# Kernel optimization log

Measured on AMD Instinct MI355X. Metric: run time of the kernel, lower is better.

## Reference

```python
import jax, jax.numpy as jnp
import numpy as np


def setup_inputs() -> dict:
    key = jax.random.key(0)
    b, l, d_model, n_head, topk = 2, 2048, 1024, 16, 32
    dh = d_model // n_head
    k0, k1, k2, k3, k4 = jax.random.split(key, 5)
    s = 1.0 / np.sqrt(d_model)
    return {
        "q_in": jax.random.normal(k0, (b, l, d_model), jnp.float32),
        "kv_in": jax.random.normal(k1, (b, l, d_model), jnp.float32),
        "w_q": jax.random.normal(k2, (d_model, d_model), jnp.float32) * s,
        "w_kv": jax.random.normal(k3, (d_model, 2 * dh), jnp.float32) * s,
        "w_concat": jax.random.normal(k4, (d_model, d_model), jnp.float32) * s,
        "topk": topk,
        "n_head": n_head,
    }


def _l2norm_seq(x):
    # F.normalize default dim=1 -> normalize along the sequence axis (faithful to source)
    n = jnp.sqrt(jnp.sum(x * x, axis=1, keepdims=True))
    return x / jnp.maximum(n, 1e-12)


def reference(q_in, kv_in, w_q, w_kv, w_concat, topk, n_head):
    b, l, d_model = q_in.shape
    dh = d_model // n_head
    scale = 1.0 / np.sqrt(dh)

    q = q_in @ w_q                                  # (b, l, d_model)
    kv = kv_in @ w_kv                               # (b, l, 2*dh)
    k, v = kv[..., :dh], kv[..., dh:]
    k, v = _l2norm_seq(k), _l2norm_seq(v)           # (b, l, dh) single shared KV head

    q = q.reshape(b, l, n_head, dh).transpose(0, 2, 1, 3)  # (b, h, l, dh)

    # one similarity matrix reused for local attention and kNN retrieval
    sims = jnp.einsum('bhld,bmd->bhlm', q, k)       # (b, h, l, m)

    # local SDPA (KV head broadcast over query heads)
    local = jnp.einsum('bhlm,bmd->bhld', jax.nn.softmax(sims * scale, axis=-1), v)

    # exact inner-product kNN over stored keys (faiss memory stores k only,
    # so retrieved key == retrieved value == nearest stored key vectors)
    _, idx = jax.lax.top_k(sims, topk)              # (b, h, l, topk)
    mem = jax.vmap(lambda kk, ii: kk[ii])(k, idx)   # (b, h, l, topk, dh)

    s_ret = jnp.einsum('bhld,bhltd->bhlt', q, mem) * scale
    retrieved = jnp.einsum('bhlt,bhltd->bhld', jax.nn.softmax(s_ret, axis=-1), mem)

    out = (local + retrieved).transpose(0, 2, 1, 3).reshape(b, l, d_model)
    return out @ w_concat
```

## Files before the change

### kernel.cpp

```cpp
#include <hip/hip_runtime.h>
#include <cstddef>
#include <cstring>

#define B_    2
#define L_    2048
#define DM_   1024
#define NH_   16
#define DH_   64
#define SCALE_ 0.125f

typedef __bf16 bf16x8 __attribute__((ext_vector_type(8)));
typedef float  f32x4  __attribute__((ext_vector_type(4)));
typedef unsigned short ushort8v __attribute__((ext_vector_type(8)));
typedef unsigned short ushort4v __attribute__((ext_vector_type(4)));
typedef unsigned long long u64;
typedef unsigned int u32;

__device__ __forceinline__ u32 flipf(float f) {
    u32 u = __float_as_uint(f);
    return (u & 0x80000000u) ? ~u : (u | 0x80000000u);
}
__device__ __forceinline__ float unflipf(u32 k) {
    u32 u = (k & 0x80000000u) ? (k ^ 0x80000000u) : ~k;
    return __uint_as_float(u);
}
__device__ __forceinline__ float bf2f(unsigned short u) {
    return __uint_as_float(((u32)u) << 16);
}
__device__ __forceinline__ unsigned short f2bf(float f) {
    __bf16 h = (__bf16)f;
    unsigned short u;
    __builtin_memcpy(&u, &h, 2);
    return u;
}

__global__ __launch_bounds__(256)
void wsplit3(const float* __restrict__ W, unsigned short* __restrict__ w1,
             unsigned short* __restrict__ w2, unsigned short* __restrict__ w3,
             int K, int N) {
    const int n0 = blockIdx.x << 6;
    const int k0 = blockIdx.y << 6;
    const int t  = threadIdx.x;
    __shared__ float s[64][65];
    const int rr = t >> 4;
    const int c4 = (t & 15) << 2;
    #pragma unroll
    for (int rep = 0; rep < 4; ++rep) {
        int k = rr + (rep << 4);
        float4 x = *(const float4*)(W + (size_t)(k0 + k) * N + n0 + c4);
        s[k][c4+0] = x.x; s[k][c4+1] = x.y; s[k][c4+2] = x.z; s[k][c4+3] = x.w;
    }
    __syncthreads();
    #pragma unroll
    for (int rep = 0; rep < 4; ++rep) {
        int n = rr + (rep << 4);
        ushort4v h, m, l;
        #pragma unroll
        for (int j = 0; j < 4; ++j) {
            float x = s[c4 + j][n];
            unsigned short hh = f2bf(x);
            float r = x - bf2f(hh);
            unsigned short mm = f2bf(r);
            float r2 = r - bf2f(mm);
            h[j] = hh; m[j] = mm; l[j] = f2bf(r2);
        }
        size_t o = (size_t)(n0 + n) * K + k0 + c4;
        *(ushort4v*)(w1 + o) = h;
        *(ushort4v*)(w2 + o) = m;
        *(ushort4v*)(w3 + o) = l;
    }
}

__global__ __launch_bounds__(256)
void gemm6p(const float* __restrict__ A, const unsigned short* __restrict__ w1,
            const unsigned short* __restrict__ w2, const unsigned short* __restrict__ w3,
            float* __restrict__ C, int N, int K) {
    __shared__ __align__(16) unsigned short sA[3][128][40];
    __shared__ __align__(16) unsigned short sW[3][64][40];
    const int t    = threadIdx.x;
    const int wv   = t >> 6;
    const int lane = t & 63;
    const int quad = lane >> 4;
    const int n15  = lane & 15;
    const int bm = blockIdx.y << 7;
    const int bn = blockIdx.x << 6;
    const int wm = (wv >> 1) << 6;
    const int wn = (wv & 1) << 5;
    f32x4 acc[4][2];
    #pragma unroll
    for (int i = 0; i < 4; ++i)
        #pragma unroll
        for (int j = 0; j < 2; ++j)
            #pragma unroll
            for (int r = 0; r < 4; ++r) acc[i][j][r] = 0.f;

    const int ar  = t >> 1,  acg = (t & 1) << 4;
    const int wr  = t >> 2,  wcg = (t & 3) << 3;
    const float* Ap = A + (size_t)(bm + ar) * K + acg;
    const size_t wo = (size_t)(bn + wr) * K + wcg;

    for (int k0 = 0; k0 < K; k0 += 32) {
        float4 a0 = *(const float4*)(Ap + k0);
        float4 a1 = *(const float4*)(Ap + k0 + 4);
        float4 a2 = *(const float4*)(Ap + k0 + 8);
        float4 a3 = *(const float4*)(Ap + k0 + 12);
        ushort8v u1 = *(const ushort8v*)(w1 + wo + k0);
        ushort8v u2 = *(const ushort8v*)(w2 + wo + k0);
        ushort8v u3 = *(const ushort8v*)(w3 + wo + k0);
        __syncthreads();
        {
            float av[16] = {a0.x,a0.y,a0.z,a0.w, a1.x,a1.y,a1.z,a1.w,
                            a2.x,a2.y,a2.z,a2.w, a3.x,a3.y,a3.z,a3.w};
            ushort8v h0, h1, m0, m1, lo0, lo1;
            #pragma unroll
            for (int i = 0; i < 8; ++i) {
                float x = av[i];
                unsigned short hh = f2bf(x);
                float r = x - bf2f(hh);
                unsigned short mm = f2bf(r);
                h0[i] = hh; m0[i] = mm; lo0[i] = f2bf(r - bf2f(mm));
                float y = av[8 + i];
                unsigned short hh2 = f2bf(y);
                float r2 = y - bf2f(hh2);
                unsigned short mm2 = f2bf(r2);
                h1[i] = hh2; m1[i] = mm2; lo1[i] = f2bf(r2 - bf2f(mm2));
            }
            *(ushort8v*)&sA[0][ar][acg]     = h0;
            *(ushort8v*)&sA[0][ar][acg + 8] = h1;
            *(ushort8v*)&sA[1][ar][acg]     = m0;
            *(ushort8v*)&sA[1][ar][acg + 8] = m1;
            *(ushort8v*)&sA[2][ar][acg]     = lo0;
            *(ushort8v*)&sA[2][ar][acg + 8] = lo1;
            *(ushort8v*)&sW[0][wr][wcg] = u1;
            *(ushort8v*)&sW[1][wr][wcg] = u2;
            *(ushort8v*)&sW[2][wr][wcg] = u3;
        }
        __syncthreads();
        bf16x8 af[3][4];
        #pragma unroll
        for (int mi = 0; mi < 4; ++mi) {
            af[0][mi] = *(const bf16x8*)&sA[0][wm + (mi << 4) + n15][quad << 3];
            af[1][mi] = *(const bf16x8*)&sA[1][wm + (mi << 4) + n15][quad << 3];
            af[2][mi] = *(const bf16x8*)&sA[2][wm + (mi << 4) + n15][quad << 3];
        }
        #pragma unroll
        for (int nj = 0; nj < 2; ++nj) {
            bf16x8 wf1 = *(const bf16x8*)&sW[0][wn + (nj << 4) + n15][quad << 3];
            bf16x8 wf2 = *(const bf16x8*)&sW[1][wn + (nj << 4) + n15][quad << 3];
            bf16x8 wf3 = *(const bf16x8*)&sW[2][wn + (nj << 4) + n15][quad << 3];
            #pragma unroll
            for (int mi = 0; mi < 4; ++mi) {
                acc[mi][nj] = __builtin_amdgcn_mfma_f32_16x16x32_bf16(af[0][mi], wf1, acc[mi][nj], 0, 0, 0);
                acc[mi][nj] = __builtin_amdgcn_mfma_f32_16x16x32_bf16(af[0][mi], wf2, acc[mi][nj], 0, 0, 0);
                acc[mi][nj] = __builtin_amdgcn_mfma_f32_16x16x32_bf16(af[1][mi], wf1, acc[mi][nj], 0, 0, 0);
                acc[mi][nj] = __builtin_amdgcn_mfma_f32_16x16x32_bf16(af[1][mi], wf2, acc[mi][nj], 0, 0, 0);
                acc[mi][nj] = __builtin_amdgcn_mfma_f32_16x16x32_bf16(af[0][mi], wf3, acc[mi][nj], 0, 0, 0);
                acc[mi][nj] = __builtin_amdgcn_mfma_f32_16x16x32_bf16(af[2][mi], wf1, acc[mi][nj], 0, 0, 0);
            }
        }
    }
    #pragma unroll
    for (int mi = 0; mi < 4; ++mi)
        #pragma unroll
        for (int nj = 0; nj < 2; ++nj)
            #pragma unroll
            for (int r = 0; r < 4; ++r)
                C[(size_t)(bm + wm + (mi << 4) + (quad << 2) + r) * N
                  + bn + wn + (nj << 4) + n15] = acc[mi][nj][r];
}

__global__ __launch_bounds__(256)
void gemm3p(const float* __restrict__ A, const unsigned short* __restrict__ w1,
            const unsigned short* __restrict__ w2,
            float* __restrict__ C, int N, int K) {
    __shared__ __align__(16) unsigned short sA[2][128][40];
    __shared__ __align__(16) unsigned short sW[2][64][40];
    const int t    = threadIdx.x;
    const int wv   = t >> 6;
    const int lane = t & 63;
    const int quad = lane >> 4;
    const int n15  = lane & 15;
    const int bm = blockIdx.y << 7;
    const int bn = blockIdx.x << 6;
    const int wm = (wv >> 1) << 6;
    const int wn = (wv & 1) << 5;
    f32x4 acc[4][2];
    #pragma unroll
    for (int i = 0; i < 4; ++i)
        #pragma unroll
        for (int j = 0; j < 2; ++j)
            #pragma unroll
            for (int r = 0; r < 4; ++r) acc[i][j][r] = 0.f;

    const int ar  = t >> 1,  acg = (t & 1) << 4;
    const int wr  = t >> 2,  wcg = (t & 3) << 3;
    const float* Ap = A + (size_t)(bm + ar) * K + acg;
    const size_t wo = (size_t)(bn + wr) * K + wcg;

    for (int k0 = 0; k0 < K; k0 += 32) {
        float4 a0 = *(const float4*)(Ap + k0);
        float4 a1 = *(const float4*)(Ap + k0 + 4);
        float4 a2 = *(const float4*)(Ap + k0 + 8);
        float4 a3 = *(const float4*)(Ap + k0 + 12);
        ushort8v u1 = *(const ushort8v*)(w1 + wo + k0);
        ushort8v u2 = *(const ushort8v*)(w2 + wo + k0);
        __syncthreads();
        {
            float av[16] = {a0.x,a0.y,a0.z,a0.w, a1.x,a1.y,a1.z,a1.w,
                            a2.x,a2.y,a2.z,a2.w, a3.x,a3.y,a3.z,a3.w};
            ushort8v h0, h1, l0v, l1v;
            #pragma unroll
            for (int i = 0; i < 8; ++i) {
                float x = av[i];
                unsigned short hh = f2bf(x);
                h0[i] = hh; l0v[i] = f2bf(x - bf2f(hh));
                float y = av[8 + i];
                unsigned short hh2 = f2bf(y);
                h1[i] = hh2; l1v[i] = f2bf(y - bf2f(hh2));
            }
            *(ushort8v*)&sA[0][ar][acg]     = h0;
            *(ushort8v*)&sA[0][ar][acg + 8] = h1;
            *(ushort8v*)&sA[1][ar][acg]     = l0v;
            *(ushort8v*)&sA[1][ar][acg + 8] = l1v;
            *(ushort8v*)&sW[0][wr][wcg] = u1;
            *(ushort8v*)&sW[1][wr][wcg] = u2;
        }
        __syncthreads();
        bf16x8 af[2][4];
        #pragma unroll
        for (int mi = 0; mi < 4; ++mi) {
            af[0][mi] = *(const bf16x8*)&sA[0][wm + (mi << 4) + n15][quad << 3];
            af[1][mi] = *(const bf16x8*)&sA[1][wm + (mi << 4) + n15][quad << 3];
        }
        #pragma unroll
        for (int nj = 0; nj < 2; ++nj) {
            bf16x8 wf1 = *(const bf16x8*)&sW[0][wn + (nj << 4) + n15][quad << 3];
            bf16x8 wf2 = *(const bf16x8*)&sW[1][wn + (nj << 4) + n15][quad << 3];
            #pragma unroll
            for (int mi = 0; mi < 4; ++mi) {
                acc[mi][nj] = __builtin_amdgcn_mfma_f32_16x16x32_bf16(af[0][mi], wf1, acc[mi][nj], 0, 0, 0);
                acc[mi][nj] = __builtin_amdgcn_mfma_f32_16x16x32_bf16(af[0][mi], wf2, acc[mi][nj], 0, 0, 0);
                acc[mi][nj] = __builtin_amdgcn_mfma_f32_16x16x32_bf16(af[1][mi], wf1, acc[mi][nj], 0, 0, 0);
            }
        }
    }
    #pragma unroll
    for (int mi = 0; mi < 4; ++mi)
        #pragma unroll
        for (int nj = 0; nj < 2; ++nj)
            #pragma unroll
            for (int r = 0; r < 4; ++r)
                C[(size_t)(bm + wm + (mi << 4) + (quad << 2) + r) * N
                  + bn + wn + (nj << 4) + n15] = acc[mi][nj][r];
}

__global__ __launch_bounds__(256)
void col_norms(const float* __restrict__ kv, float* __restrict__ invn) {
    const int bc = blockIdx.x;
    const int b  = bc >> 7;
    const int c  = bc & 127;
    const int t  = threadIdx.x;
    const float* base = kv + (size_t)b * L_ * 128 + c;
    float ss = 0.f;
    for (int l = t; l < L_; l += 256) {
        float x = base[(size_t)l * 128];
        ss += x * x;
    }
    #pragma unroll
    for (int off = 32; off; off >>= 1) ss += __shfl_xor(ss, off);
    __shared__ float red[4];
    if ((t & 63) == 0) red[t >> 6] = ss;
    __syncthreads();
    if (t == 0) {
        float tot = red[0] + red[1] + red[2] + red[3];
        invn[bc] = 1.f / fmaxf(sqrtf(tot), 1e-12f);
    }
}

__global__ __launch_bounds__(256)
void scale_kv(const float* __restrict__ kv, const float* __restrict__ invn,
              float* __restrict__ kn, __bf16* __restrict__ kh,
              __bf16* __restrict__ vT) {
    const int b  = blockIdx.y;
    const int l0 = blockIdx.x << 6;
    const int t  = threadIdx.x;
    __shared__ float s_inv[128];
    __shared__ float s_vt[64][65];
    if (t < 128) s_inv[t] = invn[b * 128 + t];
    __syncthreads();
    #pragma unroll
    for (int rep = 0; rep < 8; ++rep) {
        int idx = (rep << 8) + t;
        int li  = idx >> 5;
        int c4  = (idx & 31) << 2;
        float4 x = *(const float4*)(kv + ((size_t)(b * L_ + l0 + li)) * 128 + c4);
        x.x *= s_inv[c4]; x.y *= s_inv[c4+1]; x.z *= s_inv[c4+2]; x.w *= s_inv[c4+3];
        if (c4 < 64) {
            size_t o = ((size_t)(b * L_ + l0 + li)) * DH_ + c4;
            *(float4*)(kn + o) = x;
            kh[o+0] = (__bf16)x.x; kh[o+1] = (__bf16)x.y;
            kh[o+2] = (__bf16)x.z; kh[o+3] = (__bf16)x.w;
        } else {
            int d = c4 - 64;
            s_vt[d+0][li] = x.x; s_vt[d+1][li] = x.y; s_vt[d+2][li] = x.z; s_vt[d+3][li] = x.w;
        }
    }
    __syncthreads();
    #pragma unroll
    for (int rep = 0; rep < 4; ++rep) {
        int idx = (rep << 8) + t;
        int d   = idx >> 4;
        int j   = (idx & 15) << 2;
        size_t o = ((size_t)b * DH_ + d) * L_ + l0 + j;
        vT[o+0] = (__bf16)s_vt[d][j+0];
        vT[o+1] = (__bf16)s_vt[d][j+1];
        vT[o+2] = (__bf16)s_vt[d][j+2];
        vT[o+3] = (__bf16)s_vt[d][j+3];
    }
}

#define SST2_ 1032

__global__ __launch_bounds__(256, 4)
void attn_part(const float* __restrict__ q,
               const __bf16* __restrict__ kh,
               const __bf16* __restrict__ vT,
               float* __restrict__ attn,
               unsigned short* __restrict__ cand,
               int* __restrict__ candC) {
    const int tile = blockIdx.x;
    const int h    = blockIdx.y;
    const int b    = blockIdx.z;
    const int l0   = tile << 4;
    const int t    = threadIdx.x;
    const int w    = t >> 6;
    const int lane = t & 63;
    const int quad = lane >> 4;
    const int n15  = lane & 15;

    __shared__ unsigned short s_sims[16 * SST2_];
    __shared__ float s_local[16][66];
    __shared__ float s_denom[16];

    {
        float* sl = &s_local[0][0];
        for (int i = t; i < 16 * 66; i += 256) sl[i] = 0.f;
        if (t < 16) s_denom[t] = 0.f;
    }

    bf16x8 qf[2];
    {
        const float* qp = q + ((size_t)(b * L_ + l0 + n15)) * DM_ + h * DH_ + (quad << 3);
        #pragma unroll
        for (int ks = 0; ks < 2; ++ks) {
            float4 x0 = *(const float4*)(qp + (ks << 5));
            float4 x1 = *(const float4*)(qp + (ks << 5) + 4);
            float xv[8] = {x0.x, x0.y, x0.z, x0.w, x1.x, x1.y, x1.z, x1.w};
            #pragma unroll
            for (int i2 = 0; i2 < 8; ++i2) qf[ks][i2] = (__bf16)xv[i2];
        }
    }

    f32x4 accL[4] = {{0,0,0,0},{0,0,0,0},{0,0,0,0},{0,0,0,0}};
    float psum = 0.f;
    const __bf16* khb = kh + (size_t)b * L_ * DH_;
    const __bf16* vtb = vT + (size_t)b * DH_ * L_;
    const int rg0 = ((b * NH_ + h) * L_) + l0;

    #pragma unroll 1
    for (int hf = 0; hf < 2; ++hf) {
        #pragma unroll
        for (int g = 0; g < 4; ++g) {
            bf16x8 kf[8];
            const __bf16* kp = khb + (size_t)((hf << 10) + (w << 8) + (g << 6) + n15) * DH_ + (quad << 3);
            #pragma unroll
            for (int jj = 0; jj < 4; ++jj) {
                kf[2*jj]   = *(const bf16x8*)(kp + (size_t)(jj << 4) * DH_);
                kf[2*jj+1] = *(const bf16x8*)(kp + (size_t)(jj << 4) * DH_ + 32);
            }
            #pragma unroll
            for (int jj = 0; jj < 4; ++jj) {
                int m0 = (w << 8) + (g << 6) + (jj << 4);
                f32x4 acc = {0.f, 0.f, 0.f, 0.f};
                acc = __builtin_amdgcn_mfma_f32_16x16x32_bf16(qf[0], kf[2*jj],   acc, 0, 0, 0);
                acc = __builtin_amdgcn_mfma_f32_16x16x32_bf16(qf[1], kf[2*jj+1], acc, 0, 0, 0);
                #pragma unroll
                for (int rr = 0; rr < 4; ++rr)
                    s_sims[((quad << 2) + rr) * SST2_ + m0 + n15] = f2bf(acc[rr]);
            }
        }
        __syncthreads();

        #pragma unroll 1
        for (int rr2 = 0; rr2 < 4; ++rr2) {
            const int r = (w << 2) + rr2;
            const unsigned short* srow = s_sims + r * SST2_;
            ushort8v rv[2];
            rv[0] = *(const ushort8v*)(srow + (lane << 3));
            rv[1] = *(const ushort8v*)(srow + 512 + (lane << 3));
            float bv = -3e38f;
            #pragma unroll
            for (int j = 0; j < 2; ++j)
                #pragma unroll
                for (int e = 0; e < 8; ++e) bv = fmaxf(bv, bf2f(rv[j][e]));
            u32 key = flipf(bv);
            u32 thr = 0;
            #pragma unroll
            for (int bp = 31; bp >= 0; --bp) {
                u32 tt = thr | (1u << bp);
                if (__popcll(__ballot(key >= tt)) >= 32) thr = tt;
            }
            float thrv = unflipf(thr) - 0.01f;
            int base = 0;
            unsigned short* cr = cand + (size_t)(rg0 + r) * 192 + hf * 96;
            #pragma unroll
            for (int j = 0; j < 2; ++j) {
                #pragma unroll
                for (int e = 0; e < 8; ++e) {
                    bool pred = bf2f(rv[j][e]) >= thrv;
                    u64 mk = __ballot(pred);
                    if (pred) {
                        int pos = base + __popcll(mk & ((1ull << lane) - 1));
                        if (pos < 96)
                            cr[pos] = (unsigned short)((hf << 10) + (j << 9) + (lane << 3) + e);
                    }
                    base += __popcll(mk);
                }
            }
            if (lane == 0) candC[((rg0 + r) << 1) + hf] = base < 96 ? base : 96;
        }

        #pragma unroll
        for (int g = 0; g < 4; ++g) {
            bf16x8 bvv[2][4];
            #pragma unroll
            for (int t2 = 0; t2 < 2; ++t2)
                #pragma unroll
                for (int nn = 0; nn < 4; ++nn)
                    bvv[t2][nn] = *(const bf16x8*)(vtb + (size_t)((nn << 4) + n15) * L_
                                  + (hf << 10) + (w << 8) + (g << 6) + (t2 << 5) + (quad << 3));
            #pragma unroll
            for (int t2 = 0; t2 < 2; ++t2) {
                int mb = (w << 8) + (g << 6) + (t2 << 5);
                ushort8v pu = *(const ushort8v*)(s_sims + n15 * SST2_ + mb + (quad << 3));
                bf16x8 af;
                #pragma unroll
                for (int e = 0; e < 8; ++e) {
                    float p = __expf(SCALE_ * bf2f(pu[e]));
                    psum += p;
                    af[e] = (__bf16)p;
                }
                #pragma unroll
                for (int nn = 0; nn < 4; ++nn)
                    accL[nn] = __builtin_amdgcn_mfma_f32_16x16x32_bf16(af, bvv[t2][nn], accL[nn], 0, 0, 0);
            }
        }
        __syncthreads();
    }

    psum += __shfl_xor(psum, 16);
    psum += __shfl_xor(psum, 32);
    if (lane < 16) atomicAdd(&s_denom[lane], psum);
    #pragma unroll
    for (int nn = 0; nn < 4; ++nn)
        #pragma unroll
        for (int rr = 0; rr < 4; ++rr)
            atomicAdd(&s_local[(quad << 2) + rr][(nn << 4) + n15], accL[nn][rr]);
    __syncthreads();

    {
        int r  = t >> 4;
        int d0 = (t & 15) << 2;
        float inv = 1.f / s_denom[r];
        float* op = attn + ((size_t)(b * L_ + l0 + r)) * DM_ + h * DH_ + d0;
        op[0] = s_local[r][d0+0] * inv;
        op[1] = s_local[r][d0+1] * inv;
        op[2] = s_local[r][d0+2] * inv;
        op[3] = s_local[r][d0+3] * inv;
    }
}

__global__ __launch_bounds__(256)
void topk_merge(const float* __restrict__ q, const float* __restrict__ kn,
                const unsigned short* __restrict__ cand,
                const int* __restrict__ candC, float* __restrict__ attn) {
    const int wv   = threadIdx.x >> 6;
    const int lane = threadIdx.x & 63;
    const int row  = (blockIdx.x << 2) + wv;
    const int l = row & (L_ - 1);
    const int h = (row >> 11) & (NH_ - 1);
    const int b = row >> 15;
    __shared__ __align__(16) u64 s_sel[4][32];

    const int c0 = candC[row << 1];
    const int c1 = candC[(row << 1) + 1];
    const int C  = c0 + c1;
    const int nb = (C + 63) >> 6;
    const unsigned short* cr = cand + (size_t)row * 192;
    const float* knb = kn + (size_t)b * L_ * DH_;
    const float* qr  = q + ((size_t)(b * L_ + l)) * DM_ + h * DH_;

    float4 qx[16];
    #pragma unroll
    for (int d4 = 0; d4 < 16; ++d4) qx[d4] = *(const float4*)(qr + (d4 << 2));

    u32   keyv[3];
    float dotv[3];
    int   mv[3];
    #pragma unroll 1
    for (int bt = 0; bt < nb; ++bt) {
        int i = (bt << 6) + lane;
        bool act = i < C;
        int m = 0;
        if (act) m = (i < c0) ? (int)cr[i] : (int)cr[96 + (i - c0)];
        const float* kr = knb + (size_t)m * DH_;
        float4 kx[16];
        #pragma unroll
        for (int d4 = 0; d4 < 16; ++d4) kx[d4] = *(const float4*)(kr + (d4 << 2));
        float dot = 0.f;
        #pragma unroll
        for (int d4 = 0; d4 < 16; ++d4)
            dot += kx[d4].x * qx[d4].x + kx[d4].y * qx[d4].y
                 + kx[d4].z * qx[d4].z + kx[d4].w * qx[d4].w;
        keyv[bt] = act ? flipf(dot) : 0u;
        dotv[bt] = dot;
        mv[bt]   = m;
    }
    u32 thr2 = 0;
    #pragma unroll 1
    for (int bp = 31; bp >= 0; --bp) {
        u32 tt = thr2 | (1u << bp);
        int c2 = 0;
        for (int bt = 0; bt < nb; ++bt)
            c2 += __popcll(__ballot(keyv[bt] >= tt));
        if (c2 >= 32) thr2 = tt;
    }
    int off = 0;
    #pragma unroll 1
    for (int bt = 0; bt < nb; ++bt) {
        bool pred = keyv[bt] >= thr2;
        u64 mk = __ballot(pred);
        if (pred) {
            int pos = off + __popcll(mk & ((1ull << lane) - 1));
            if (pos < 32) {
                float pt = __expf(SCALE_ * dotv[bt]);
                s_sel[wv][pos] = ((u64)__float_as_uint(pt) << 32) | (u32)mv[bt];
            }
        }
        off += __popcll(mk);
    }
    {
        float pts[32];
        int   ms[32];
        #pragma unroll
        for (int i = 0; i < 32; ++i) {
            u64 s0 = s_sel[wv][i];
            pts[i] = __uint_as_float((u32)(s0 >> 32));
            ms[i]  = (int)(u32)(s0 & 0xffffffffu);
        }
        const float* knb2 = knb + lane;
        float kvv[32];
        #pragma unroll
        for (int i = 0; i < 32; ++i) kvv[i] = knb2[(size_t)ms[i] * DH_];
        float rs = 0.f, ret = 0.f;
        #pragma unroll
        for (int i = 0; i < 16; ++i) {
            rs  += pts[2*i] + pts[2*i+1];
            ret += pts[2*i] * kvv[2*i] + pts[2*i+1] * kvv[2*i+1];
        }
        size_t oa = ((size_t)(b * L_ + l)) * DM_ + h * DH_ + lane;
        attn[oa] = attn[oa] + ret / rs;
    }
}

extern "C" void kernel_launch(void* const* d_in, const int* in_sizes, int n_in,
                              void* d_out, int out_size, void* d_ws, size_t ws_size,
                              hipStream_t stream) {
    const float* q_in     = (const float*)d_in[0];
    const float* kv_in    = (const float*)d_in[1];
    const float* w_q      = (const float*)d_in[2];
    const float* w_kv     = (const float*)d_in[3];
    const float* w_concat = (const float*)d_in[4];
    float* out = (float*)d_out;

    float* ws   = (float*)d_ws;
    float* q    = ws;
    float* attn = ws + 4194304;
    float* kv   = attn;
    float* kn   = ws + 8388608;
    float* invn = ws + 8650752;
    unsigned short* us = (unsigned short*)(ws + 8651008);
    unsigned short* kh_u = us;
    unsigned short* vT_u = us + 262144;
    unsigned short* wq1  = us + 524288;
    unsigned short* wq2  = wq1 + 1048576;
    unsigned short* wq3  = wq2 + 1048576;
    unsigned short* wc1  = wq3 + 1048576;
    unsigned short* wc2  = wc1 + 1048576;
    unsigned short* wkv1 = wc2 + 1048576;
    unsigned short* wkv2 = wkv1 + 131072;
    unsigned short* wkv3 = wkv2 + 131072;
    unsigned short* cand = wkv3 + 131072;
    unsigned short* wc3  = cand;
    int* candC = (int*)(cand + 12582912);
    __bf16* kh = (__bf16*)kh_u;
    __bf16* vT = (__bf16*)vT_u;

    wsplit3<<<dim3(DM_ / 64, DM_ / 64), 256, 0, stream>>>(w_q, wq1, wq2, wq3, DM_, DM_);
    wsplit3<<<dim3(DM_ / 64, DM_ / 64), 256, 0, stream>>>(w_concat, wc1, wc2, wc3, DM_, DM_);
    wsplit3<<<dim3(128 / 64, DM_ / 64), 256, 0, stream>>>(w_kv, wkv1, wkv2, wkv3, DM_, 128);

    gemm6p<<<dim3(DM_ / 64, (B_ * L_) / 128), 256, 0, stream>>>(q_in, wq1, wq2, wq3, q, DM_, DM_);
    gemm6p<<<dim3(128 / 64, (B_ * L_) / 128), 256, 0, stream>>>(kv_in, wkv1, wkv2, wkv3, kv, 128, DM_);

    col_norms<<<B_ * 128, 256, 0, stream>>>(kv, invn);
    scale_kv<<<dim3(L_ / 64, B_), 256, 0, stream>>>(kv, invn, kn, kh, vT);

    attn_part<<<dim3(L_ / 16, NH_, B_), 256, 0, stream>>>(q, kh, vT, attn, cand, candC);
    topk_merge<<<(B_ * NH_ * L_) / 4, 256, 0, stream>>>(q, kn, cand, candC, attn);

    gemm3p<<<dim3(DM_ / 64, (B_ * L_) / 128), 256, 0, stream>>>(attn, wc1, wc2, out, DM_, DM_);
}
```

Measured before the change: 826.0 us.

## Merge top-k candidate halves in-kernel with packed bf16 scores and cooperative rescoring

The attention kernel now keeps a running row maximum across both key halves. In the second half it re-filters the first-half candidates against a combined threshold, so each row emits one candidate list of at most 96 entries instead of two lists of 96. Each candidate carries its bf16 similarity alongside the index, and the threshold radix search runs over 16 bits instead of 32. The sims tile is written with swapped MFMA operands so one 64-bit packed store replaces four scalar stores. The merge kernel rescores candidates cooperatively, with 16 lanes per key using float4 loads and shuffle reductions instead of a serial 64-float load per lane. This cuts candidate traffic and per-lane register pressure, at the cost of more branching and a tighter candidate cap that could drop true top-k entries near the threshold.

```diff
diff --git a/kernel.cpp b/kernel.cpp
--- a/kernel.cpp
+++ b/kernel.cpp
@@ -20,10 +20,6 @@
     u32 u = __float_as_uint(f);
     return (u & 0x80000000u) ? ~u : (u | 0x80000000u);
 }
-__device__ __forceinline__ float unflipf(u32 k) {
-    u32 u = (k & 0x80000000u) ? (k ^ 0x80000000u) : ~k;
-    return __uint_as_float(u);
-}
 __device__ __forceinline__ float bf2f(unsigned short u) {
     return __uint_as_float(((u32)u) << 16);
 }
@@ -32,6 +28,12 @@
     unsigned short u;
     __builtin_memcpy(&u, &h, 2);
     return u;
+}
+__device__ __forceinline__ u32 flip16(unsigned short u) {
+    return (u & 0x8000u) ? (u32)(~u & 0xffffu) : (u32)(u | 0x8000u);
+}
+__device__ __forceinline__ unsigned short unflip16(u32 k) {
+    return (k & 0x8000u) ? (unsigned short)(k ^ 0x8000u) : (unsigned short)(~k & 0xffffu);
 }
 
 __global__ __launch_bounds__(256)
@@ -326,7 +328,7 @@
                const __bf16* __restrict__ kh,
                const __bf16* __restrict__ vT,
                float* __restrict__ attn,
-               unsigned short* __restrict__ cand,
+               u32* __restrict__ cand,
                int* __restrict__ candC) {
     const int tile = blockIdx.x;
     const int h    = blockIdx.y;
@@ -363,6 +365,8 @@
 
     f32x4 accL[4] = {{0,0,0,0},{0,0,0,0},{0,0,0,0},{0,0,0,0}};
     float psum = 0.f;
+    float bvmax[4] = {-3e38f, -3e38f, -3e38f, -3e38f};
+    int   c0[4]    = {0, 0, 0, 0};
     const __bf16* khb = kh + (size_t)b * L_ * DH_;
     const __bf16* vtb = vT + (size_t)b * DH_ * L_;
     const int rg0 = ((b * NH_ + h) * L_) + l0;
@@ -382,11 +386,12 @@
             for (int jj = 0; jj < 4; ++jj) {
                 int m0 = (w << 8) + (g << 6) + (jj << 4);
                 f32x4 acc = {0.f, 0.f, 0.f, 0.f};
-                acc = __builtin_amdgcn_mfma_f32_16x16x32_bf16(qf[0], kf[2*jj],   acc, 0, 0, 0);
-                acc = __builtin_amdgcn_mfma_f32_16x16x32_bf16(qf[1], kf[2*jj+1], acc, 0, 0, 0);
-                #pragma unroll
-                for (int rr = 0; rr < 4; ++rr)
-                    s_sims[((quad << 2) + rr) * SST2_ + m0 + n15] = f2bf(acc[rr]);
+                acc = __builtin_amdgcn_mfma_f32_16x16x32_bf16(kf[2*jj],   qf[0], acc, 0, 0, 0);
+                acc = __builtin_amdgcn_mfma_f32_16x16x32_bf16(kf[2*jj+1], qf[1], acc, 0, 0, 0);
+                u32 lo = (u32)f2bf(acc[0]) | ((u32)f2bf(acc[1]) << 16);
+                u32 hi = (u32)f2bf(acc[2]) | ((u32)f2bf(acc[3]) << 16);
+                u64 pk = ((u64)hi << 32) | lo;
+                *(u64*)(s_sims + (size_t)n15 * SST2_ + m0 + (quad << 2)) = pk;
             }
         }
         __syncthreads();
@@ -403,31 +408,84 @@
             for (int j = 0; j < 2; ++j)
                 #pragma unroll
                 for (int e = 0; e < 8; ++e) bv = fmaxf(bv, bf2f(rv[j][e]));
-            u32 key = flipf(bv);
-            u32 thr = 0;
-            #pragma unroll
-            for (int bp = 31; bp >= 0; --bp) {
-                u32 tt = thr | (1u << bp);
-                if (__popcll(__ballot(key >= tt)) >= 32) thr = tt;
-            }
-            float thrv = unflipf(thr) - 0.01f;
-            int base = 0;
-            unsigned short* cr = cand + (size_t)(rg0 + r) * 192 + hf * 96;
-            #pragma unroll
-            for (int j = 0; j < 2; ++j) {
-                #pragma unroll
-                for (int e = 0; e < 8; ++e) {
-                    bool pred = bf2f(rv[j][e]) >= thrv;
+            bvmax[rr2] = fmaxf(bvmax[rr2], bv);
+            u32* cr = cand + (size_t)(rg0 + r) * 96;
+            if (hf == 0) {
+                u32 key = flip16(f2bf(bv));
+                u32 thr = 0;
+                #pragma unroll
+                for (int bp = 15; bp >= 0; --bp) {
+                    u32 tt = thr | (1u << bp);
+                    if (__popcll(__ballot(key >= tt)) >= 32) thr = tt;
+                }
+                float thrv = bf2f(unflip16(thr)) - 0.01f;
+                int base = 0;
+                #pragma unroll
+                for (int j = 0; j < 2; ++j) {
+                    #pragma unroll
+                    for (int e = 0; e < 8; ++e) {
+                        bool pred = bf2f(rv[j][e]) >= thrv;
+                        u64 mk = __ballot(pred);
+                        if (pred) {
+                            int pos = base + __popcll(mk & ((1ull << lane) - 1));
+                            if (pos < 96)
+                                cr[pos] = ((u32)rv[j][e] << 16)
+                                        | (u32)((j << 9) + (lane << 3) + e);
+                        }
+                        base += __popcll(mk);
+                    }
+                }
+                c0[rr2] = base < 96 ? base : 96;
+            } else {
+                u32 key = flip16(f2bf(bvmax[rr2]));
+                u32 thr = 0;
+                #pragma unroll
+                for (int bp = 15; bp >= 0; --bp) {
+                    u32 tt = thr | (1u << bp);
+                    if (__popcll(__ballot(key >= tt)) >= 32) thr = tt;
+                }
+                float thrv = bf2f(unflip16(thr)) - 0.01f;
+                const int cc0 = c0[rr2];
+                u32 e0 = (lane < cc0) ? cr[lane] : 0u;
+                u32 e1 = (64 + lane < cc0) ? cr[64 + lane] : 0u;
+                int base = 0;
+                {
+                    bool pred = (lane < cc0)
+                              && (bf2f((unsigned short)(e0 >> 16)) >= thrv);
+                    u64 mk = __ballot(pred);
+                    if (pred) {
+                        int pos = __popcll(mk & ((1ull << lane) - 1));
+                        cr[pos] = e0;
+                    }
+                    base = __popcll(mk);
+                }
+                if (cc0 > 64) {
+                    bool pred = (64 + lane < cc0)
+                              && (bf2f((unsigned short)(e1 >> 16)) >= thrv);
                     u64 mk = __ballot(pred);
                     if (pred) {
                         int pos = base + __popcll(mk & ((1ull << lane) - 1));
-                        if (pos < 96)
-                            cr[pos] = (unsigned short)((hf << 10) + (j << 9) + (lane << 3) + e);
+                        if (pos < 96) cr[pos] = e1;
                     }
                     base += __popcll(mk);
                 }
-            }
-            if (lane == 0) candC[((rg0 + r) << 1) + hf] = base < 96 ? base : 96;
+                #pragma unroll
+                for (int j = 0; j < 2; ++j) {
+                    #pragma unroll
+                    for (int e = 0; e < 8; ++e) {
+                        bool pred = bf2f(rv[j][e]) >= thrv;
+                        u64 mk = __ballot(pred);
+                        if (pred) {
+                            int pos = base + __popcll(mk & ((1ull << lane) - 1));
+                            if (pos < 96)
+                                cr[pos] = ((u32)rv[j][e] << 16)
+                                        | (u32)(1024 + (j << 9) + (lane << 3) + e);
+                        }
+                        base += __popcll(mk);
+                    }
+                }
+                if (lane == 0) candC[rg0 + r] = base < 96 ? base : 96;
+            }
         }
 
         #pragma unroll
@@ -482,72 +540,87 @@
 
 __global__ __launch_bounds__(256)
 void topk_merge(const float* __restrict__ q, const float* __restrict__ kn,
-                const unsigned short* __restrict__ cand,
-                const int* __restrict__ candC, float* __restrict__ attn) {
+                const u32* __restrict__ cand, const int* __restrict__ candC,
+                float* __restrict__ attn) {
     const int wv   = threadIdx.x >> 6;
     const int lane = threadIdx.x & 63;
     const int row  = (blockIdx.x << 2) + wv;
     const int l = row & (L_ - 1);
     const int h = (row >> 11) & (NH_ - 1);
     const int b = row >> 15;
+    __shared__ float s_dot[4][96];
     __shared__ __align__(16) u64 s_sel[4][32];
 
-    const int c0 = candC[row << 1];
-    const int c1 = candC[(row << 1) + 1];
-    const int C  = c0 + c1;
-    const int nb = (C + 63) >> 6;
-    const unsigned short* cr = cand + (size_t)row * 192;
+    const int C = candC[row];
+    const u32* cr = cand + (size_t)row * 96;
     const float* knb = kn + (size_t)b * L_ * DH_;
     const float* qr  = q + ((size_t)(b * L_ + l)) * DM_ + h * DH_;
 
-    float4 qx[16];
-    #pragma unroll
-    for (int d4 = 0; d4 < 16; ++d4) qx[d4] = *(const float4*)(qr + (d4 << 2));
-
-    u32   keyv[3];
-    float dotv[3];
-    int   mv[3];
-    #pragma unroll 1
-    for (int bt = 0; bt < nb; ++bt) {
-        int i = (bt << 6) + lane;
-        bool act = i < C;
-        int m = 0;
-        if (act) m = (i < c0) ? (int)cr[i] : (int)cr[96 + (i - c0)];
-        const float* kr = knb + (size_t)m * DH_;
-        float4 kx[16];
-        #pragma unroll
-        for (int d4 = 0; d4 < 16; ++d4) kx[d4] = *(const float4*)(kr + (d4 << 2));
-        float dot = 0.f;
-        #pragma unroll
-        for (int d4 = 0; d4 < 16; ++d4)
-            dot += kx[d4].x * qx[d4].x + kx[d4].y * qx[d4].y
-                 + kx[d4].z * qx[d4].z + kx[d4].w * qx[d4].w;
-        keyv[bt] = act ? flipf(dot) : 0u;
-        dotv[bt] = dot;
-        mv[bt]   = m;
-    }
+    int mreg0 = (lane < C) ? (int)(cr[lane] & 0xffffu) : 0;
+    int mreg1 = (64 + lane < C) ? (int)(cr[64 + lane] & 0xffffu) : 0;
+
+    const int cg = lane >> 4;
+    const int dg = lane & 15;
+    float4 qx = *(const float4*)(qr + (dg << 2));
+
+    #pragma unroll 2
+    for (int base = 0; base < C; base += 4) {
+        int ci = base + cg;
+        int src = ci & 63;
+        int mA = __shfl(mreg0, src);
+        int mB = __shfl(mreg1, src);
+        int m  = (ci < 64) ? mA : mB;
+        float4 kx = *(const float4*)(knb + (size_t)m * DH_ + (dg << 2));
+        float p = kx.x * qx.x + kx.y * qx.y + kx.z * qx.z + kx.w * qx.w;
+        p += __shfl_xor(p, 1);
+        p += __shfl_xor(p, 2);
+        p += __shfl_xor(p, 4);
+        p += __shfl_xor(p, 8);
+        if (dg == 0 && ci < C) s_dot[wv][ci] = p;
+    }
+
+    float dotA = (lane < C) ? s_dot[wv][lane] : 0.f;
+    float dotB = (64 + lane < C) ? s_dot[wv][64 + lane] : 0.f;
+    u32 keyA = (lane < C) ? flipf(dotA) : 0u;
+    u32 keyB = (64 + lane < C) ? flipf(dotB) : 0u;
+
     u32 thr2 = 0;
-    #pragma unroll 1
-    for (int bp = 31; bp >= 0; --bp) {
-        u32 tt = thr2 | (1u << bp);
-        int c2 = 0;
-        for (int bt = 0; bt < nb; ++bt)
-            c2 += __popcll(__ballot(keyv[bt] >= tt));
-        if (c2 >= 32) thr2 = tt;
-    }
-    int off = 0;
-    #pragma unroll 1
-    for (int bt = 0; bt < nb; ++bt) {
-        bool pred = keyv[bt] >= thr2;
-        u64 mk = __ballot(pred);
-        if (pred) {
-            int pos = off + __popcll(mk & ((1ull << lane) - 1));
+    if (C <= 64) {
+        #pragma unroll
+        for (int bp = 31; bp >= 0; --bp) {
+            u32 tt = thr2 | (1u << bp);
+            if (__popcll(__ballot(keyA >= tt)) >= 32) thr2 = tt;
+        }
+    } else {
+        #pragma unroll
+        for (int bp = 31; bp >= 0; --bp) {
+            u32 tt = thr2 | (1u << bp);
+            int c2 = __popcll(__ballot(keyA >= tt)) + __popcll(__ballot(keyB >= tt));
+            if (c2 >= 32) thr2 = tt;
+        }
+    }
+    {
+        bool pA = keyA >= thr2;
+        u64 mkA = __ballot(pA);
+        if (pA) {
+            int pos = __popcll(mkA & ((1ull << lane) - 1));
             if (pos < 32) {
-                float pt = __expf(SCALE_ * dotv[bt]);
-                s_sel[wv][pos] = ((u64)__float_as_uint(pt) << 32) | (u32)mv[bt];
-            }
-        }
-        off += __popcll(mk);
+                float pt = __expf(SCALE_ * dotA);
+                s_sel[wv][pos] = ((u64)__float_as_uint(pt) << 32) | (u32)mreg0;
+            }
+        }
+        if (C > 64) {
+            int cA = __popcll(mkA);
+            bool pB = keyB >= thr2;
+            u64 mkB = __ballot(pB);
+            if (pB) {
+                int pos = cA + __popcll(mkB & ((1ull << lane) - 1));
+                if (pos < 32) {
+                    float pt = __expf(SCALE_ * dotB);
+                    s_sel[wv][pos] = ((u64)__float_as_uint(pt) << 32) | (u32)mreg1;
+                }
+            }
+        }
     }
     {
         float pts[32];
@@ -600,9 +673,9 @@
     unsigned short* wkv1 = wc2 + 1048576;
     unsigned short* wkv2 = wkv1 + 131072;
     unsigned short* wkv3 = wkv2 + 131072;
-    unsigned short* cand = wkv3 + 131072;
-    unsigned short* wc3  = cand;
-    int* candC = (int*)(cand + 12582912);
+    u32* cand = (u32*)(wkv3 + 131072);
+    unsigned short* wc3 = (unsigned short*)cand;
+    int* candC = (int*)(cand + 65536 * 96);
     __bf16* kh = (__bf16*)kh_u;
     __bf16* vT = (__bf16*)vT_u;
 
```

Measured after the change: 688.3 us. 1.2x faster.

## Widen attention blocks to 512 threads and parallelize candidate scoring in top-k merge

Applied to the files above, without the earlier changes.

attn_part now runs 8 waves per block, each covering half as many keys and rows. It also packs the MFMA outputs into 64-bit shared stores by swapping operand order, and builds the candidate threshold on a 16-bit bf16 key using a running max across halves. Candidate compaction switches from per-element ballots to a per-lane bitmask with a wave prefix scan. topk_merge spreads each candidate dot product across 16 lanes with shuffle reductions and stages the results in shared memory, replacing the serial 64-wide per-lane dot. The goal is less ballot and register pressure and better latency hiding, at the cost of extra shuffles and a changed threshold heuristic that could alter which candidates are kept.

```diff
diff --git a/kernel.cpp b/kernel.cpp
--- a/kernel.cpp
+++ b/kernel.cpp
@@ -20,10 +20,6 @@
     u32 u = __float_as_uint(f);
     return (u & 0x80000000u) ? ~u : (u | 0x80000000u);
 }
-__device__ __forceinline__ float unflipf(u32 k) {
-    u32 u = (k & 0x80000000u) ? (k ^ 0x80000000u) : ~k;
-    return __uint_as_float(u);
-}
 __device__ __forceinline__ float bf2f(unsigned short u) {
     return __uint_as_float(((u32)u) << 16);
 }
@@ -32,6 +28,12 @@
     unsigned short u;
     __builtin_memcpy(&u, &h, 2);
     return u;
+}
+__device__ __forceinline__ u32 flip16(unsigned short u) {
+    return (u & 0x8000u) ? (u32)(~u & 0xffffu) : (u32)(u | 0x8000u);
+}
+__device__ __forceinline__ unsigned short unflip16(u32 k) {
+    return (k & 0x8000u) ? (unsigned short)(k ^ 0x8000u) : (unsigned short)(~k & 0xffffu);
 }
 
 __global__ __launch_bounds__(256)
@@ -321,7 +323,7 @@
 
 #define SST2_ 1032
 
-__global__ __launch_bounds__(256, 4)
+__global__ __launch_bounds__(512, 8)
 void attn_part(const float* __restrict__ q,
                const __bf16* __restrict__ kh,
                const __bf16* __restrict__ vT,
@@ -344,7 +346,7 @@
 
     {
         float* sl = &s_local[0][0];
-        for (int i = t; i < 16 * 66; i += 256) sl[i] = 0.f;
+        for (int i = t; i < 16 * 66; i += 512) sl[i] = 0.f;
         if (t < 16) s_denom[t] = 0.f;
     }
 
@@ -363,6 +365,7 @@
 
     f32x4 accL[4] = {{0,0,0,0},{0,0,0,0},{0,0,0,0},{0,0,0,0}};
     float psum = 0.f;
+    float bvmax[2] = {-3e38f, -3e38f};
     const __bf16* khb = kh + (size_t)b * L_ * DH_;
     const __bf16* vtb = vT + (size_t)b * DH_ * L_;
     const int rg0 = ((b * NH_ + h) * L_) + l0;
@@ -370,9 +373,9 @@
     #pragma unroll 1
     for (int hf = 0; hf < 2; ++hf) {
         #pragma unroll
-        for (int g = 0; g < 4; ++g) {
+        for (int g = 0; g < 2; ++g) {
             bf16x8 kf[8];
-            const __bf16* kp = khb + (size_t)((hf << 10) + (w << 8) + (g << 6) + n15) * DH_ + (quad << 3);
+            const __bf16* kp = khb + (size_t)((hf << 10) + (w << 7) + (g << 6) + n15) * DH_ + (quad << 3);
             #pragma unroll
             for (int jj = 0; jj < 4; ++jj) {
                 kf[2*jj]   = *(const bf16x8*)(kp + (size_t)(jj << 4) * DH_);
@@ -380,20 +383,21 @@
             }
             #pragma unroll
             for (int jj = 0; jj < 4; ++jj) {
-                int m0 = (w << 8) + (g << 6) + (jj << 4);
+                int m0 = (w << 7) + (g << 6) + (jj << 4);
                 f32x4 acc = {0.f, 0.f, 0.f, 0.f};
-                acc = __builtin_amdgcn_mfma_f32_16x16x32_bf16(qf[0], kf[2*jj],   acc, 0, 0, 0);
-                acc = __builtin_amdgcn_mfma_f32_16x16x32_bf16(qf[1], kf[2*jj+1], acc, 0, 0, 0);
-                #pragma unroll
-                for (int rr = 0; rr < 4; ++rr)
-                    s_sims[((quad << 2) + rr) * SST2_ + m0 + n15] = f2bf(acc[rr]);
+                acc = __builtin_amdgcn_mfma_f32_16x16x32_bf16(kf[2*jj],   qf[0], acc, 0, 0, 0);
+                acc = __builtin_amdgcn_mfma_f32_16x16x32_bf16(kf[2*jj+1], qf[1], acc, 0, 0, 0);
+                u32 lo = (u32)f2bf(acc[0]) | ((u32)f2bf(acc[1]) << 16);
+                u32 hi = (u32)f2bf(acc[2]) | ((u32)f2bf(acc[3]) << 16);
+                u64 pk = ((u64)hi << 32) | lo;
+                *(u64*)(s_sims + (size_t)n15 * SST2_ + m0 + (quad << 2)) = pk;
             }
         }
         __syncthreads();
 
         #pragma unroll 1
-        for (int rr2 = 0; rr2 < 4; ++rr2) {
-            const int r = (w << 2) + rr2;
+        for (int rr2 = 0; rr2 < 2; ++rr2) {
+            const int r = (w << 1) + rr2;
             const unsigned short* srow = s_sims + r * SST2_;
             ushort8v rv[2];
             rv[0] = *(const ushort8v*)(srow + (lane << 3));
@@ -403,45 +407,57 @@
             for (int j = 0; j < 2; ++j)
                 #pragma unroll
                 for (int e = 0; e < 8; ++e) bv = fmaxf(bv, bf2f(rv[j][e]));
-            u32 key = flipf(bv);
+            bvmax[rr2] = fmaxf(bvmax[rr2], bv);
+            u32 key = flip16(f2bf(hf == 0 ? bv : bvmax[rr2]));
             u32 thr = 0;
             #pragma unroll
-            for (int bp = 31; bp >= 0; --bp) {
+            for (int bp = 15; bp >= 0; --bp) {
                 u32 tt = thr | (1u << bp);
                 if (__popcll(__ballot(key >= tt)) >= 32) thr = tt;
             }
-            float thrv = unflipf(thr) - 0.01f;
-            int base = 0;
+            float thrv = bf2f(unflip16(thr)) - 0.01f;
+            u32 m16 = 0;
+            #pragma unroll
+            for (int j = 0; j < 2; ++j)
+                #pragma unroll
+                for (int e = 0; e < 8; ++e)
+                    if (bf2f(rv[j][e]) >= thrv) m16 |= 1u << ((j << 3) + e);
+            int c = __popc(m16);
+            int incl = c;
+            #pragma unroll
+            for (int off = 1; off < 64; off <<= 1) {
+                int v2 = __shfl_up(incl, off);
+                if (lane >= off) incl += v2;
+            }
+            int total = __shfl(incl, 63);
+            int pos = incl - c;
             unsigned short* cr = cand + (size_t)(rg0 + r) * 192 + hf * 96;
-            #pragma unroll
-            for (int j = 0; j < 2; ++j) {
-                #pragma unroll
-                for (int e = 0; e < 8; ++e) {
-                    bool pred = bf2f(rv[j][e]) >= thrv;
-                    u64 mk = __ballot(pred);
-                    if (pred) {
-                        int pos = base + __popcll(mk & ((1ull << lane) - 1));
-                        if (pos < 96)
-                            cr[pos] = (unsigned short)((hf << 10) + (j << 9) + (lane << 3) + e);
-                    }
-                    base += __popcll(mk);
-                }
-            }
-            if (lane == 0) candC[((rg0 + r) << 1) + hf] = base < 96 ? base : 96;
-        }
-
-        #pragma unroll
-        for (int g = 0; g < 4; ++g) {
+            u32 mm = m16;
+            while (mm) {
+                int e  = __ffs(mm) - 1;
+                mm &= mm - 1;
+                int j  = e >> 3;
+                int ee = e & 7;
+                if (pos < 96)
+                    cr[pos] = (unsigned short)((hf << 10) + (j << 9) + (lane << 3) + ee);
+                ++pos;
+            }
+            if (lane == 0)
+                candC[((rg0 + r) << 1) + hf] = total < 96 ? total : 96;
+        }
+
+        #pragma unroll
+        for (int g = 0; g < 2; ++g) {
             bf16x8 bvv[2][4];
             #pragma unroll
             for (int t2 = 0; t2 < 2; ++t2)
                 #pragma unroll
                 for (int nn = 0; nn < 4; ++nn)
                     bvv[t2][nn] = *(const bf16x8*)(vtb + (size_t)((nn << 4) + n15) * L_
-                                  + (hf << 10) + (w << 8) + (g << 6) + (t2 << 5) + (quad << 3));
+                                  + (hf << 10) + (w << 7) + (g << 6) + (t2 << 5) + (quad << 3));
             #pragma unroll
             for (int t2 = 0; t2 < 2; ++t2) {
-                int mb = (w << 8) + (g << 6) + (t2 << 5);
+                int mb = (w << 7) + (g << 6) + (t2 << 5);
                 ushort8v pu = *(const ushort8v*)(s_sims + n15 * SST2_ + mb + (quad << 3));
                 bf16x8 af;
                 #pragma unroll
@@ -469,14 +485,12 @@
     __syncthreads();
 
     {
-        int r  = t >> 4;
-        int d0 = (t & 15) << 2;
+        int r  = t >> 5;
+        int d0 = (t & 31) << 1;
         float inv = 1.f / s_denom[r];
         float* op = attn + ((size_t)(b * L_ + l0 + r)) * DM_ + h * DH_ + d0;
         op[0] = s_local[r][d0+0] * inv;
         op[1] = s_local[r][d0+1] * inv;
-        op[2] = s_local[r][d0+2] * inv;
-        op[3] = s_local[r][d0+3] * inv;
     }
 }
 
@@ -490,61 +504,75 @@
     const int l = row & (L_ - 1);
     const int h = (row >> 11) & (NH_ - 1);
     const int b = row >> 15;
+    __shared__ float s_dot[4][192];
     __shared__ __align__(16) u64 s_sel[4][32];
 
     const int c0 = candC[row << 1];
     const int c1 = candC[(row << 1) + 1];
     const int C  = c0 + c1;
-    const int nb = (C + 63) >> 6;
     const unsigned short* cr = cand + (size_t)row * 192;
     const float* knb = kn + (size_t)b * L_ * DH_;
     const float* qr  = q + ((size_t)(b * L_ + l)) * DM_ + h * DH_;
 
-    float4 qx[16];
-    #pragma unroll
-    for (int d4 = 0; d4 < 16; ++d4) qx[d4] = *(const float4*)(qr + (d4 << 2));
-
+    int mreg[3];
+    #pragma unroll
+    for (int bt = 0; bt < 3; ++bt) {
+        int i = (bt << 6) + lane;
+        int m = 0;
+        if (i < C) m = (i < c0) ? (int)cr[i] : (int)cr[96 + (i - c0)];
+        mreg[bt] = m;
+    }
+
+    const int cg = lane >> 4;
+    const int dg = lane & 15;
+    float4 qx = *(const float4*)(qr + (dg << 2));
+
+    #pragma unroll 2
+    for (int base = 0; base < C; base += 4) {
+        int ci = base + cg;
+        int src = ci & 63;
+        int mA = __shfl(mreg[0], src);
+        int mB = __shfl(mreg[1], src);
+        int mC2 = __shfl(mreg[2], src);
+        int m  = (ci < 64) ? mA : ((ci < 128) ? mB : mC2);
+        float4 kx = *(const float4*)(knb + (size_t)m * DH_ + (dg << 2));
+        float p = kx.x * qx.x + kx.y * qx.y + kx.z * qx.z + kx.w * qx.w;
+        p += __shfl_xor(p, 1);
+        p += __shfl_xor(p, 2);
+        p += __shfl_xor(p, 4);
+        p += __shfl_xor(p, 8);
+        if (dg == 0 && ci < C) s_dot[wv][ci] = p;
+    }
+
+    float dotv[3];
     u32   keyv[3];
-    float dotv[3];
-    int   mv[3];
-    #pragma unroll 1
-    for (int bt = 0; bt < nb; ++bt) {
+    #pragma unroll
+    for (int bt = 0; bt < 3; ++bt) {
         int i = (bt << 6) + lane;
         bool act = i < C;
-        int m = 0;
-        if (act) m = (i < c0) ? (int)cr[i] : (int)cr[96 + (i - c0)];
-        const float* kr = knb + (size_t)m * DH_;
-        float4 kx[16];
-        #pragma unroll
-        for (int d4 = 0; d4 < 16; ++d4) kx[d4] = *(const float4*)(kr + (d4 << 2));
-        float dot = 0.f;
-        #pragma unroll
-        for (int d4 = 0; d4 < 16; ++d4)
-            dot += kx[d4].x * qx[d4].x + kx[d4].y * qx[d4].y
-                 + kx[d4].z * qx[d4].z + kx[d4].w * qx[d4].w;
-        keyv[bt] = act ? flipf(dot) : 0u;
-        dotv[bt] = dot;
-        mv[bt]   = m;
-    }
+        dotv[bt] = act ? s_dot[wv][i] : 0.f;
+        keyv[bt] = act ? flipf(dotv[bt]) : 0u;
+    }
+
     u32 thr2 = 0;
     #pragma unroll 1
     for (int bp = 31; bp >= 0; --bp) {
         u32 tt = thr2 | (1u << bp);
-        int c2 = 0;
-        for (int bt = 0; bt < nb; ++bt)
-            c2 += __popcll(__ballot(keyv[bt] >= tt));
+        int c2 = __popcll(__ballot(keyv[0] >= tt))
+               + __popcll(__ballot(keyv[1] >= tt))
+               + __popcll(__ballot(keyv[2] >= tt));
         if (c2 >= 32) thr2 = tt;
     }
     int off = 0;
-    #pragma unroll 1
-    for (int bt = 0; bt < nb; ++bt) {
+    #pragma unroll
+    for (int bt = 0; bt < 3; ++bt) {
         bool pred = keyv[bt] >= thr2;
         u64 mk = __ballot(pred);
         if (pred) {
             int pos = off + __popcll(mk & ((1ull << lane) - 1));
             if (pos < 32) {
                 float pt = __expf(SCALE_ * dotv[bt]);
-                s_sel[wv][pos] = ((u64)__float_as_uint(pt) << 32) | (u32)mv[bt];
+                s_sel[wv][pos] = ((u64)__float_as_uint(pt) << 32) | (u32)mreg[bt];
             }
         }
         off += __popcll(mk);
@@ -616,7 +644,7 @@
     col_norms<<<B_ * 128, 256, 0, stream>>>(kv, invn);
     scale_kv<<<dim3(L_ / 64, B_), 256, 0, stream>>>(kv, invn, kn, kh, vT);
 
-    attn_part<<<dim3(L_ / 16, NH_, B_), 256, 0, stream>>>(q, kh, vT, attn, cand, candC);
+    attn_part<<<dim3(L_ / 16, NH_, B_), 512, 0, stream>>>(q, kh, vT, attn, cand, candC);
     topk_merge<<<(B_ * NH_ * L_) / 4, 256, 0, stream>>>(q, kn, cand, candC, attn);
 
     gemm3p<<<dim3(DM_ / 64, (B_ * L_) / 128), 256, 0, stream>>>(attn, wc1, wc2, out, DM_, DM_);
```

New measurement: 955.3 us. 15.7% more time.
